# Kernel optimization log

Hardware: AMD Instinct MI355X
Metric: run time of the kernel (lower is better)

Reference implementation:

```python
import jax, jax.numpy as jnp
import numpy as np

NUM_EXPERTS = 8
TOP_K = 2
HIDDEN = 1024
INTER = 3584
BATCH = 2
SEQ = 2048
TOKENS = BATCH * SEQ


def setup_inputs() -> dict:
    key = jax.random.key(0)
    k_h, k_l, k_w1, k_w2, k_w3 = jax.random.split(key, 5)
    hidden_states = jax.random.normal(k_h, (TOKENS, HIDDEN), dtype=jnp.float32)
    # Router: top-2 over softmaxed logits, renormalized (standard Mixtral routing)
    logits = jax.random.normal(k_l, (TOKENS, NUM_EXPERTS), dtype=jnp.float32)
    probs = jax.nn.softmax(logits, axis=-1)
    routing_weights, selected = jax.lax.top_k(probs, TOP_K)  # [T, K], [T, K]
    routing_weights = routing_weights / jnp.sum(routing_weights, axis=-1, keepdims=True)
    # expert_mask: [num_experts, top_k, tokens]
    expert_mask = jax.nn.one_hot(selected, NUM_EXPERTS, dtype=jnp.int32).transpose(2, 1, 0)
    scale = 0.02
    w1 = jax.random.normal(k_w1, (NUM_EXPERTS, HIDDEN, INTER), dtype=jnp.float32) * scale
    w2 = jax.random.normal(k_w2, (NUM_EXPERTS, INTER, HIDDEN), dtype=jnp.float32) * scale
    w3 = jax.random.normal(k_w3, (NUM_EXPERTS, HIDDEN, INTER), dtype=jnp.float32) * scale
    return {
        "expert_mask": expert_mask,
        "hidden_states": hidden_states,
        "routing_weights": routing_weights,
        "w1": w1,
        "w2": w2,
        "w3": w3,
        "batch_size": BATCH,
        "sequence_length": SEQ,
        "hidden_dim": HIDDEN,
    }


def reference(expert_mask, hidden_states, routing_weights, w1, w2, w3,
              batch_size, sequence_length, hidden_dim):
    num_experts = w1.shape[0]
    tokens = batch_size * sequence_length
    # Extra row at the end absorbs writes from fill_value=-1 padding (as in source).
    final = jnp.zeros((tokens + 1, hidden_dim), dtype=hidden_states.dtype)
    for e in range(num_experts):
        # idx: which top-k slot; top_x: which token. Padded with -1.
        idx, top_x = jnp.nonzero(expert_mask[e], size=sequence_length, fill_value=-1)
        cur = hidden_states[top_x]  # [S, H]
        h = (jax.nn.silu(cur @ w1[e]) * (cur @ w3[e])) @ w2[e]  # SwiGLU MLP
        h = h * routing_weights[top_x, idx, None]
        final = final.at[top_x].set(h + final[top_x])
    final = final[:-1]
    return final.reshape(batch_size, sequence_length, hidden_dim)
```

## Files before the change

kernel.cpp:

```cpp
#include <hip/hip_runtime.h>
#include <hip/hip_bf16.h>
#include <cstdint>
#include <cstddef>

#define NEXP  8
#define NTOK  4096
#define HID   1024
#define INTER 3584
#define CAP   2048

#define BM  128
#define BN  128
#define BK  32

typedef __attribute__((ext_vector_type(4))) float floatx4;
typedef __attribute__((ext_vector_type(8))) short shortx8;
typedef unsigned short u16;

__device__ __forceinline__ u16 f2bf(float f) {
    union { float f; unsigned u; } v; v.f = f;
    unsigned r = v.u + 0x7fffu + ((v.u >> 16) & 1u);
    return (u16)(r >> 16);
}

__device__ __forceinline__ shortx8 pack8(const float* v) {
    shortx8 r;
#pragma unroll
    for (int i = 0; i < 8; ++i) r[i] = (short)f2bf(v[i]);
    return r;
}

__device__ __forceinline__ void async_ld16(const void* g, void* l) {
    __builtin_amdgcn_global_load_lds(
        (const __attribute__((address_space(1))) unsigned int*)g,
        (__attribute__((address_space(3))) unsigned int*)l, 16, 0, 0);
}

__global__ void route_kernel(const int* __restrict__ mask, const float* __restrict__ rw,
                             int* __restrict__ cnt, int* __restrict__ list,
                             float* __restrict__ wgt) {
    int t = blockIdx.x * blockDim.x + threadIdx.x;
    if (t >= NTOK) return;
#pragma unroll
    for (int e = 0; e < NEXP; ++e) {
#pragma unroll
        for (int k = 0; k < 2; ++k) {
            if (mask[(e * 2 + k) * NTOK + t] != 0) {
                int pos = atomicAdd(&cnt[e], 1);
                if (pos < CAP) {
                    list[e * CAP + pos] = t;
                    wgt[e * CAP + pos] = rw[t * 2 + k];
                }
            }
        }
    }
}

__global__ void xcvt_kernel(const float* __restrict__ X, u16* __restrict__ Xb) {
    const int i = (blockIdx.x * 256 + threadIdx.x) * 8;
    float4 a = *(const float4*)&X[i];
    float4 b = *(const float4*)&X[i + 4];
    float v[8] = {a.x, a.y, a.z, a.w, b.x, b.y, b.z, b.w};
    *(shortx8*)&Xb[i] = pack8(v);
}

__global__ void transpose_cvt_kernel(const float* __restrict__ src, u16* __restrict__ dst,
                                     int K, int N) {
    const int e = blockIdx.z;
    src += (size_t)e * K * N;
    dst += (size_t)e * K * N;
    const int n0 = blockIdx.x * 64;
    const int k0 = blockIdx.y * 64;
    __shared__ u16 lds[64 * 72];
    const int t  = threadIdx.x;
    const int rr = t >> 4;
    const int c4 = t & 15;
#pragma unroll
    for (int it = 0; it < 4; ++it) {
        const int r = it * 16 + rr;
        float4 f = *(const float4*)&src[(size_t)(k0 + r) * N + n0 + c4 * 4];
        lds[(c4 * 4 + 0) * 72 + r] = f2bf(f.x);
        lds[(c4 * 4 + 1) * 72 + r] = f2bf(f.y);
        lds[(c4 * 4 + 2) * 72 + r] = f2bf(f.z);
        lds[(c4 * 4 + 3) * 72 + r] = f2bf(f.w);
    }
    __syncthreads();
    const int row8 = t >> 3;
    const int col8 = t & 7;
#pragma unroll
    for (int it = 0; it < 2; ++it) {
        const int row = it * 32 + row8;
        *(shortx8*)&dst[(size_t)(n0 + row) * K + k0 + col8 * 8] =
            *(const shortx8*)&lds[row * 72 + col8 * 8];
    }
}

__global__ __launch_bounds__(256, 2)
void gemm1_kernel(const u16* __restrict__ Xb, const u16* __restrict__ W1b,
                  const u16* __restrict__ W3b, const int* __restrict__ cnt,
                  const int* __restrict__ list, const float* __restrict__ wgt,
                  u16* __restrict__ H) {
    const int e  = blockIdx.z;
    const int ce = min(cnt[e], CAP);
    const int m0 = blockIdx.y * BM;
    if (m0 >= ce) return;
    const int n0 = blockIdx.x * BN;

    __shared__ u16 lA [BM * BK];
    __shared__ u16 lB1[BN * BK];
    __shared__ u16 lB3[BN * BK];

    const int tid  = threadIdx.x;
    const int lane = tid & 63;
    const int wave = tid >> 6;

    const int srow0 = wave * 32 + (lane >> 2);
    const int srow1 = srow0 + 16;
    const int scol  = (lane & 3) * 8;
    const int lo0 = wave * 1024 + lane * 8;
    const int lo1 = lo0 + 512;

    const int t0 = list[e * CAP + min(m0 + srow0, ce - 1)];
    const int t1 = list[e * CAP + min(m0 + srow1, ce - 1)];
    const u16* ap0  = Xb + (size_t)t0 * HID + scol;
    const u16* ap1  = Xb + (size_t)t1 * HID + scol;
    const u16* b1p0 = W1b + ((size_t)e * INTER + n0 + srow0) * HID + scol;
    const u16* b1p1 = b1p0 + (size_t)16 * HID;
    const u16* b3p0 = W3b + ((size_t)e * INTER + n0 + srow0) * HID + scol;
    const u16* b3p1 = b3p0 + (size_t)16 * HID;

    const int fl = lane & 15, fq = lane >> 4;
    const int wm  = (wave >> 1) * 64;
    const int wnn = (wave & 1) * 64;

    floatx4 acc1[4][4], acc3[4][4];
#pragma unroll
    for (int i = 0; i < 4; ++i)
#pragma unroll
        for (int j = 0; j < 4; ++j)
#pragma unroll
            for (int r = 0; r < 4; ++r) { acc1[i][j][r] = 0.f; acc3[i][j][r] = 0.f; }

    for (int k0 = 0; k0 < HID; k0 += BK) {
        __syncthreads();
        async_ld16(ap0  + k0, &lA [lo0]);
        async_ld16(ap1  + k0, &lA [lo1]);
        async_ld16(b1p0 + k0, &lB1[lo0]);
        async_ld16(b1p1 + k0, &lB1[lo1]);
        async_ld16(b3p0 + k0, &lB3[lo0]);
        async_ld16(b3p1 + k0, &lB3[lo1]);
        __syncthreads();

        shortx8 af[4], b1f[4], b3f[4];
#pragma unroll
        for (int i = 0; i < 4; ++i)
            af[i] = *(const shortx8*)&lA[(wm + i * 16 + fl) * BK + fq * 8];
#pragma unroll
        for (int j = 0; j < 4; ++j) {
            b1f[j] = *(const shortx8*)&lB1[(wnn + j * 16 + fl) * BK + fq * 8];
            b3f[j] = *(const shortx8*)&lB3[(wnn + j * 16 + fl) * BK + fq * 8];
        }
#pragma unroll
        for (int i = 0; i < 4; ++i)
#pragma unroll
            for (int j = 0; j < 4; ++j) {
                acc1[i][j] = __builtin_amdgcn_mfma_f32_16x16x32_bf16(af[i], b1f[j], acc1[i][j], 0, 0, 0);
                acc3[i][j] = __builtin_amdgcn_mfma_f32_16x16x32_bf16(af[i], b3f[j], acc3[i][j], 0, 0, 0);
            }
    }

#pragma unroll
    for (int i = 0; i < 4; ++i) {
        const int rowb = m0 + wm + i * 16 + fq * 4;
#pragma unroll
        for (int r = 0; r < 4; ++r) {
            const int row = rowb + r;
            const bool valid = row < ce;
            const float rwv = valid ? wgt[e * CAP + row] : 0.f;
            u16* hp = H + (size_t)(e * CAP + (valid ? row : 0)) * INTER;
#pragma unroll
            for (int j = 0; j < 4; ++j) {
                const int col = n0 + wnn + j * 16 + fl;
                float h1 = acc1[i][j][r];
                float h3 = acc3[i][j][r];
                float sv = h1 / (1.f + __expf(-h1)) * h3 * rwv;
                if (valid) hp[col] = f2bf(sv);
            }
        }
    }
}

__global__ __launch_bounds__(256, 2)
void gemm2_kernel(const u16* __restrict__ H, const u16* __restrict__ W2b,
                  const int* __restrict__ cnt, const int* __restrict__ list,
                  float* __restrict__ out) {
    const int e  = blockIdx.z;
    const int ce = min(cnt[e], CAP);
    const int m0 = blockIdx.y * BM;
    if (m0 >= ce) return;
    const int n0 = blockIdx.x * BN;

    __shared__ u16 lA[BM * BK];
    __shared__ u16 lB[BN * BK];

    const int tid  = threadIdx.x;
    const int lane = tid & 63;
    const int wave = tid >> 6;

    const int srow0 = wave * 32 + (lane >> 2);
    const int srow1 = srow0 + 16;
    const int scol  = (lane & 3) * 8;
    const int lo0 = wave * 1024 + lane * 8;
    const int lo1 = lo0 + 512;

    const u16* ap0 = H + (size_t)(e * CAP + m0 + srow0) * INTER + scol;
    const u16* ap1 = ap0 + (size_t)16 * INTER;
    const u16* bp0 = W2b + ((size_t)e * HID + n0 + srow0) * INTER + scol;
    const u16* bp1 = bp0 + (size_t)16 * INTER;

    const int fl = lane & 15, fq = lane >> 4;
    const int wm  = (wave >> 1) * 64;
    const int wnn = (wave & 1) * 64;

    floatx4 acc[4][4];
#pragma unroll
    for (int i = 0; i < 4; ++i)
#pragma unroll
        for (int j = 0; j < 4; ++j)
#pragma unroll
            for (int r = 0; r < 4; ++r) acc[i][j][r] = 0.f;

    for (int k0 = 0; k0 < INTER; k0 += BK) {
        __syncthreads();
        async_ld16(ap0 + k0, &lA[lo0]);
        async_ld16(ap1 + k0, &lA[lo1]);
        async_ld16(bp0 + k0, &lB[lo0]);
        async_ld16(bp1 + k0, &lB[lo1]);
        __syncthreads();

        shortx8 af[4], bf[4];
#pragma unroll
        for (int i = 0; i < 4; ++i)
            af[i] = *(const shortx8*)&lA[(wm + i * 16 + fl) * BK + fq * 8];
#pragma unroll
        for (int j = 0; j < 4; ++j)
            bf[j] = *(const shortx8*)&lB[(wnn + j * 16 + fl) * BK + fq * 8];
#pragma unroll
        for (int i = 0; i < 4; ++i)
#pragma unroll
            for (int j = 0; j < 4; ++j)
                acc[i][j] = __builtin_amdgcn_mfma_f32_16x16x32_bf16(af[i], bf[j], acc[i][j], 0, 0, 0);
    }

#pragma unroll
    for (int i = 0; i < 4; ++i) {
        const int rowb = m0 + wm + i * 16 + fq * 4;
#pragma unroll
        for (int r = 0; r < 4; ++r) {
            const int row = rowb + r;
            const bool valid = row < ce;
            const int tok = valid ? list[e * CAP + row] : 0;
            float* op = out + (size_t)tok * HID;
#pragma unroll
            for (int j = 0; j < 4; ++j) {
                const int col = n0 + wnn + j * 16 + fl;
                if (valid) atomicAdd(&op[col], acc[i][j][r]);
            }
        }
    }
}

extern "C" void kernel_launch(void* const* d_in, const int* in_sizes, int n_in,
                              void* d_out, int out_size, void* d_ws, size_t ws_size,
                              hipStream_t stream) {
    const int*   mask = (const int*)  d_in[0];
    const float* X    = (const float*)d_in[1];
    const float* rw   = (const float*)d_in[2];
    const float* w1   = (const float*)d_in[3];
    const float* w2   = (const float*)d_in[4];
    const float* w3   = (const float*)d_in[5];
    float* out = (float*)d_out;

    char* ws = (char*)d_ws;
    size_t off = 0;
    int*   cnt  = (int*)(ws + off);  off += 256;
    int*   list = (int*)(ws + off);  off += (size_t)NEXP * CAP * 4;
    float* wgt  = (float*)(ws + off); off += (size_t)NEXP * CAP * 4;
    u16*   Xb   = (u16*)(ws + off);  off += (size_t)NTOK * HID * 2;
    u16*   W1b  = (u16*)(ws + off);  off += (size_t)NEXP * HID * INTER * 2;
    u16*   W3b  = (u16*)(ws + off);  off += (size_t)NEXP * HID * INTER * 2;
    u16*   W2b  = (u16*)(ws + off);  off += (size_t)NEXP * HID * INTER * 2;
    u16*   H    = (u16*)(ws + off);  off += (size_t)NEXP * CAP * INTER * 2;

    hipMemsetAsync(cnt, 0, 256, stream);
    hipMemsetAsync(d_out, 0, (size_t)out_size * sizeof(float), stream);

    route_kernel<<<dim3((NTOK + 255) / 256), dim3(256), 0, stream>>>(mask, rw, cnt, list, wgt);
    xcvt_kernel<<<dim3(NTOK * HID / (256 * 8)), dim3(256), 0, stream>>>(X, Xb);
    transpose_cvt_kernel<<<dim3(INTER / 64, HID / 64, NEXP), dim3(256), 0, stream>>>(w1, W1b, HID, INTER);
    transpose_cvt_kernel<<<dim3(INTER / 64, HID / 64, NEXP), dim3(256), 0, stream>>>(w3, W3b, HID, INTER);
    transpose_cvt_kernel<<<dim3(HID / 64, INTER / 64, NEXP), dim3(256), 0, stream>>>(w2, W2b, INTER, HID);

    gemm1_kernel<<<dim3(INTER / BN, CAP / BM, NEXP), dim3(256), 0, stream>>>(Xb, W1b, W3b, cnt, list, wgt, H);
    gemm2_kernel<<<dim3(HID / BN, CAP / BM, NEXP), dim3(256), 0, stream>>>(H, W2b, cnt, list, out);
}
```

Before: 722.8 us.

## Enlarge GEMM M-tile, XCD-aware block mapping, replace atomics with partials plus combine

The GEMM M-tile doubles to 256 rows and blocks grow to 512 threads (8 waves), so each weight tile is reused across more tokens. Blocks use a flattened grid that maps experts and column tiles onto XCDs for L2 locality. The scatter atomicAdd in gemm2 is replaced by plain stores into a per-slot partial buffer that aliases the W1b region, followed by a combine kernel that sums each token's two slots, which also drops the output memset. The weight transpose kernels are merged and pack two bf16 values per 32-bit LDS word. The aliasing of part onto W1b depends on W1b no longer being needed after gemm1, and the larger tiles raise register and LDS pressure.

```diff
diff --git a/kernel.cpp b/kernel.cpp
--- a/kernel.cpp
+++ b/kernel.cpp
@@ -9,13 +9,14 @@
 #define INTER 3584
 #define CAP   2048
 
-#define BM  128
+#define BM  256
 #define BN  128
 #define BK  32
 
 typedef __attribute__((ext_vector_type(4))) float floatx4;
 typedef __attribute__((ext_vector_type(8))) short shortx8;
 typedef unsigned short u16;
+typedef unsigned int   u32;
 
 __device__ __forceinline__ u16 f2bf(float f) {
     union { float f; unsigned u; } v; v.f = f;
@@ -38,7 +39,7 @@
 
 __global__ void route_kernel(const int* __restrict__ mask, const float* __restrict__ rw,
                              int* __restrict__ cnt, int* __restrict__ list,
-                             float* __restrict__ wgt) {
+                             float* __restrict__ wgt, int* __restrict__ slot) {
     int t = blockIdx.x * blockDim.x + threadIdx.x;
     if (t >= NTOK) return;
 #pragma unroll
@@ -50,6 +51,9 @@
                 if (pos < CAP) {
                     list[e * CAP + pos] = t;
                     wgt[e * CAP + pos] = rw[t * 2 + k];
+                    slot[t * 2 + k] = e * CAP + pos;
+                } else {
+                    slot[t * 2 + k] = -1;
                 }
             }
         }
@@ -64,47 +68,71 @@
     *(shortx8*)&Xb[i] = pack8(v);
 }
 
-__global__ void transpose_cvt_kernel(const float* __restrict__ src, u16* __restrict__ dst,
-                                     int K, int N) {
+__device__ __forceinline__ void tcvt_tile(const float* __restrict__ src, u16* __restrict__ dst,
+                                          int K, int N, int n0, int k0, u32* ldsT, int t) {
+    const int nc  = t & 15;
+    const int kp0 = t >> 4;
+#pragma unroll
+    for (int it = 0; it < 2; ++it) {
+        const int kp = kp0 + it * 16;
+        const int k  = kp * 2;
+        const float* s0 = src + (size_t)(k0 + k) * N + n0 + nc * 4;
+        float4 f0 = *(const float4*)s0;
+        float4 f1 = *(const float4*)(s0 + N);
+        ldsT[(nc * 4 + 0) * 33 + kp] = (u32)f2bf(f0.x) | ((u32)f2bf(f1.x) << 16);
+        ldsT[(nc * 4 + 1) * 33 + kp] = (u32)f2bf(f0.y) | ((u32)f2bf(f1.y) << 16);
+        ldsT[(nc * 4 + 2) * 33 + kp] = (u32)f2bf(f0.z) | ((u32)f2bf(f1.z) << 16);
+        ldsT[(nc * 4 + 3) * 33 + kp] = (u32)f2bf(f0.w) | ((u32)f2bf(f1.w) << 16);
+    }
+    __syncthreads();
+    const int rr = t >> 3;
+    const int c  = t & 7;
+#pragma unroll
+    for (int it = 0; it < 2; ++it) {
+        const int n = rr + it * 32;
+        const u32* p = &ldsT[n * 33 + c * 4];
+        u32 v0 = p[0], v1 = p[1], v2 = p[2], v3 = p[3];
+        u32* d = (u32*)&dst[(size_t)(n0 + n) * K + k0 + c * 8];
+        d[0] = v0; d[1] = v1; d[2] = v2; d[3] = v3;
+    }
+}
+
+__global__ __launch_bounds__(256)
+void tcvt13_kernel(const float* __restrict__ w1, const float* __restrict__ w3,
+                   u16* __restrict__ W1b, u16* __restrict__ W3b) {
+    __shared__ u32 ldsT[64 * 33];
+    const int z = blockIdx.z;
+    const int e = z >> 1;
+    const float* src = ((z & 1) ? w3 : w1) + (size_t)e * HID * INTER;
+    u16*         dst = ((z & 1) ? W3b : W1b) + (size_t)e * HID * INTER;
+    tcvt_tile(src, dst, HID, INTER, blockIdx.x * 64, blockIdx.y * 64, ldsT, threadIdx.x);
+}
+
+__global__ __launch_bounds__(256)
+void tcvt2_kernel(const float* __restrict__ w2, u16* __restrict__ W2b) {
+    __shared__ u32 ldsT[64 * 33];
     const int e = blockIdx.z;
-    src += (size_t)e * K * N;
-    dst += (size_t)e * K * N;
-    const int n0 = blockIdx.x * 64;
-    const int k0 = blockIdx.y * 64;
-    __shared__ u16 lds[64 * 72];
-    const int t  = threadIdx.x;
-    const int rr = t >> 4;
-    const int c4 = t & 15;
-#pragma unroll
-    for (int it = 0; it < 4; ++it) {
-        const int r = it * 16 + rr;
-        float4 f = *(const float4*)&src[(size_t)(k0 + r) * N + n0 + c4 * 4];
-        lds[(c4 * 4 + 0) * 72 + r] = f2bf(f.x);
-        lds[(c4 * 4 + 1) * 72 + r] = f2bf(f.y);
-        lds[(c4 * 4 + 2) * 72 + r] = f2bf(f.z);
-        lds[(c4 * 4 + 3) * 72 + r] = f2bf(f.w);
-    }
-    __syncthreads();
-    const int row8 = t >> 3;
-    const int col8 = t & 7;
-#pragma unroll
-    for (int it = 0; it < 2; ++it) {
-        const int row = it * 32 + row8;
-        *(shortx8*)&dst[(size_t)(n0 + row) * K + k0 + col8 * 8] =
-            *(const shortx8*)&lds[row * 72 + col8 * 8];
-    }
-}
-
-__global__ __launch_bounds__(256, 2)
+    tcvt_tile(w2 + (size_t)e * INTER * HID, W2b + (size_t)e * INTER * HID,
+              INTER, HID, blockIdx.x * 64, blockIdx.y * 64, ldsT, threadIdx.x);
+}
+
+__global__ __launch_bounds__(512, 2)
 void gemm1_kernel(const u16* __restrict__ Xb, const u16* __restrict__ W1b,
                   const u16* __restrict__ W3b, const int* __restrict__ cnt,
                   const int* __restrict__ list, const float* __restrict__ wgt,
                   u16* __restrict__ H) {
-    const int e  = blockIdx.z;
-    const int ce = min(cnt[e], CAP);
-    const int m0 = blockIdx.y * BM;
+    const int f = blockIdx.x;
+    const int xcd = f & 7;
+    const int u   = f >> 3;
+    const int mb  = u & 7;
+    const int p   = u >> 3;
+    const int pair = xcd * 28 + p;
+    const int nb  = pair % 28;
+    const int e   = pair / 28;
+    const int ce  = min(cnt[e], CAP);
+    const int m0  = mb * BM;
     if (m0 >= ce) return;
-    const int n0 = blockIdx.x * BN;
+    const int n0  = nb * BN;
 
     __shared__ u16 lA [BM * BK];
     __shared__ u16 lB1[BN * BK];
@@ -113,21 +141,20 @@
     const int tid  = threadIdx.x;
     const int lane = tid & 63;
     const int wave = tid >> 6;
-
-    const int srow0 = wave * 32 + (lane >> 2);
-    const int srow1 = srow0 + 16;
-    const int scol  = (lane & 3) * 8;
-    const int lo0 = wave * 1024 + lane * 8;
-    const int lo1 = lo0 + 512;
-
-    const int t0 = list[e * CAP + min(m0 + srow0, ce - 1)];
-    const int t1 = list[e * CAP + min(m0 + srow1, ce - 1)];
-    const u16* ap0  = Xb + (size_t)t0 * HID + scol;
-    const u16* ap1  = Xb + (size_t)t1 * HID + scol;
-    const u16* b1p0 = W1b + ((size_t)e * INTER + n0 + srow0) * HID + scol;
-    const u16* b1p1 = b1p0 + (size_t)16 * HID;
-    const u16* b3p0 = W3b + ((size_t)e * INTER + n0 + srow0) * HID + scol;
-    const u16* b3p1 = b3p0 + (size_t)16 * HID;
+    const int rsub = lane >> 2;
+    const int scol = (lane & 3) * 8;
+
+    const int arow0 = wave * 32 + rsub;
+    const int aoff0 = wave * 1024 + lane * 8;
+    const int aoff1 = aoff0 + 512;
+    const int t0 = list[e * CAP + min(m0 + arow0, ce - 1)];
+    const int t1 = list[e * CAP + min(m0 + arow0 + 16, ce - 1)];
+    const u16* ap0 = Xb + (size_t)t0 * HID + scol;
+    const u16* ap1 = Xb + (size_t)t1 * HID + scol;
+    const int brow = wave * 16 + rsub;
+    const int boff = wave * 512 + lane * 8;
+    const u16* b1p = W1b + ((size_t)e * INTER + n0 + brow) * HID + scol;
+    const u16* b3p = W3b + ((size_t)e * INTER + n0 + brow) * HID + scol;
 
     const int fl = lane & 15, fq = lane >> 4;
     const int wm  = (wave >> 1) * 64;
@@ -143,12 +170,10 @@
 
     for (int k0 = 0; k0 < HID; k0 += BK) {
         __syncthreads();
-        async_ld16(ap0  + k0, &lA [lo0]);
-        async_ld16(ap1  + k0, &lA [lo1]);
-        async_ld16(b1p0 + k0, &lB1[lo0]);
-        async_ld16(b1p1 + k0, &lB1[lo1]);
-        async_ld16(b3p0 + k0, &lB3[lo0]);
-        async_ld16(b3p1 + k0, &lB3[lo1]);
+        async_ld16(ap0 + k0, &lA [aoff0]);
+        async_ld16(ap1 + k0, &lA [aoff1]);
+        async_ld16(b1p + k0, &lB1[boff]);
+        async_ld16(b3p + k0, &lB3[boff]);
         __syncthreads();
 
         shortx8 af[4], b1f[4], b3f[4];
@@ -190,15 +215,21 @@
     }
 }
 
-__global__ __launch_bounds__(256, 2)
+__global__ __launch_bounds__(512, 2)
 void gemm2_kernel(const u16* __restrict__ H, const u16* __restrict__ W2b,
-                  const int* __restrict__ cnt, const int* __restrict__ list,
-                  float* __restrict__ out) {
-    const int e  = blockIdx.z;
-    const int ce = min(cnt[e], CAP);
-    const int m0 = blockIdx.y * BM;
+                  const int* __restrict__ cnt, float* __restrict__ part) {
+    const int f = blockIdx.x;
+    const int xcd = f & 7;
+    const int u   = f >> 3;
+    const int mb  = u & 7;
+    const int p   = u >> 3;
+    const int pair = xcd * 8 + p;
+    const int nb  = pair & 7;
+    const int e   = pair >> 3;
+    const int ce  = min(cnt[e], CAP);
+    const int m0  = mb * BM;
     if (m0 >= ce) return;
-    const int n0 = blockIdx.x * BN;
+    const int n0  = nb * BN;
 
     __shared__ u16 lA[BM * BK];
     __shared__ u16 lB[BN * BK];
@@ -206,17 +237,17 @@
     const int tid  = threadIdx.x;
     const int lane = tid & 63;
     const int wave = tid >> 6;
-
-    const int srow0 = wave * 32 + (lane >> 2);
-    const int srow1 = srow0 + 16;
-    const int scol  = (lane & 3) * 8;
-    const int lo0 = wave * 1024 + lane * 8;
-    const int lo1 = lo0 + 512;
-
-    const u16* ap0 = H + (size_t)(e * CAP + m0 + srow0) * INTER + scol;
+    const int rsub = lane >> 2;
+    const int scol = (lane & 3) * 8;
+
+    const int arow0 = wave * 32 + rsub;
+    const int aoff0 = wave * 1024 + lane * 8;
+    const int aoff1 = aoff0 + 512;
+    const u16* ap0 = H + (size_t)(e * CAP + m0 + arow0) * INTER + scol;
     const u16* ap1 = ap0 + (size_t)16 * INTER;
-    const u16* bp0 = W2b + ((size_t)e * HID + n0 + srow0) * INTER + scol;
-    const u16* bp1 = bp0 + (size_t)16 * INTER;
+    const int brow = wave * 16 + rsub;
+    const int boff = wave * 512 + lane * 8;
+    const u16* bp = W2b + ((size_t)e * HID + n0 + brow) * INTER + scol;
 
     const int fl = lane & 15, fq = lane >> 4;
     const int wm  = (wave >> 1) * 64;
@@ -232,10 +263,9 @@
 
     for (int k0 = 0; k0 < INTER; k0 += BK) {
         __syncthreads();
-        async_ld16(ap0 + k0, &lA[lo0]);
-        async_ld16(ap1 + k0, &lA[lo1]);
-        async_ld16(bp0 + k0, &lB[lo0]);
-        async_ld16(bp1 + k0, &lB[lo1]);
+        async_ld16(ap0 + k0, &lA[aoff0]);
+        async_ld16(ap1 + k0, &lA[aoff1]);
+        async_ld16(bp  + k0, &lB[boff]);
         __syncthreads();
 
         shortx8 af[4], bf[4];
@@ -259,15 +289,33 @@
         for (int r = 0; r < 4; ++r) {
             const int row = rowb + r;
             const bool valid = row < ce;
-            const int tok = valid ? list[e * CAP + row] : 0;
-            float* op = out + (size_t)tok * HID;
+            float* pp = part + (size_t)(e * CAP + row) * HID;
 #pragma unroll
             for (int j = 0; j < 4; ++j) {
                 const int col = n0 + wnn + j * 16 + fl;
-                if (valid) atomicAdd(&op[col], acc[i][j][r]);
+                if (valid) pp[col] = acc[i][j][r];
             }
         }
     }
+}
+
+__global__ void combine_kernel(const float* __restrict__ part, const int* __restrict__ slot,
+                               float* __restrict__ out) {
+    const int gid = blockIdx.x * 256 + threadIdx.x;
+    const int t = gid >> 8;
+    const int h = (gid & 255) * 4;
+    const int s0 = slot[t * 2];
+    const int s1 = slot[t * 2 + 1];
+    float4 r = make_float4(0.f, 0.f, 0.f, 0.f);
+    if (s0 >= 0) {
+        float4 a = *(const float4*)&part[(size_t)s0 * HID + h];
+        r.x += a.x; r.y += a.y; r.z += a.z; r.w += a.w;
+    }
+    if (s1 >= 0) {
+        float4 b = *(const float4*)&part[(size_t)s1 * HID + h];
+        r.x += b.x; r.y += b.y; r.z += b.z; r.w += b.w;
+    }
+    *(float4*)&out[(size_t)t * HID + h] = r;
 }
 
 extern "C" void kernel_launch(void* const* d_in, const int* in_sizes, int n_in,
@@ -283,24 +331,27 @@
 
     char* ws = (char*)d_ws;
     size_t off = 0;
-    int*   cnt  = (int*)(ws + off);  off += 256;
-    int*   list = (int*)(ws + off);  off += (size_t)NEXP * CAP * 4;
+    int*   cnt  = (int*)(ws + off);   off += 256;
+    int*   list = (int*)(ws + off);   off += (size_t)NEXP * CAP * 4;
     float* wgt  = (float*)(ws + off); off += (size_t)NEXP * CAP * 4;
-    u16*   Xb   = (u16*)(ws + off);  off += (size_t)NTOK * HID * 2;
-    u16*   W1b  = (u16*)(ws + off);  off += (size_t)NEXP * HID * INTER * 2;
-    u16*   W3b  = (u16*)(ws + off);  off += (size_t)NEXP * HID * INTER * 2;
-    u16*   W2b  = (u16*)(ws + off);  off += (size_t)NEXP * HID * INTER * 2;
-    u16*   H    = (u16*)(ws + off);  off += (size_t)NEXP * CAP * INTER * 2;
+    int*   slot = (int*)(ws + off);   off += (size_t)NTOK * 2 * 4;
+    u16*   Xb   = (u16*)(ws + off);   off += (size_t)NTOK * HID * 2;
+    u16*   W1b  = (u16*)(ws + off);   off += (size_t)NEXP * HID * INTER * 2;
+    u16*   W3b  = (u16*)(ws + off);   off += (size_t)NEXP * HID * INTER * 2;
+    u16*   W2b  = (u16*)(ws + off);   off += (size_t)NEXP * HID * INTER * 2;
+    u16*   H    = (u16*)(ws + off);   off += (size_t)NEXP * CAP * INTER * 2;
+    float* part = (float*)W1b;
 
     hipMemsetAsync(cnt, 0, 256, stream);
-    hipMemsetAsync(d_out, 0, (size_t)out_size * sizeof(float), stream);
-
-    route_kernel<<<dim3((NTOK + 255) / 256), dim3(256), 0, stream>>>(mask, rw, cnt, list, wgt);
+
+    route_kernel<<<dim3((NTOK + 255) / 256), dim3(256), 0, stream>>>(mask, rw, cnt, list, wgt, slot);
     xcvt_kernel<<<dim3(NTOK * HID / (256 * 8)), dim3(256), 0, stream>>>(X, Xb);
-    transpose_cvt_kernel<<<dim3(INTER / 64, HID / 64, NEXP), dim3(256), 0, stream>>>(w1, W1b, HID, INTER);
-    transpose_cvt_kernel<<<dim3(INTER / 64, HID / 64, NEXP), dim3(256), 0, stream>>>(w3, W3b, HID, INTER);
-    transpose_cvt_kernel<<<dim3(HID / 64, INTER / 64, NEXP), dim3(256), 0, stream>>>(w2, W2b, INTER, HID);
-
-    gemm1_kernel<<<dim3(INTER / BN, CAP / BM, NEXP), dim3(256), 0, stream>>>(Xb, W1b, W3b, cnt, list, wgt, H);
-    gemm2_kernel<<<dim3(HID / BN, CAP / BM, NEXP), dim3(256), 0, stream>>>(H, W2b, cnt, list, out);
-}
+    tcvt13_kernel<<<dim3(INTER / 64, HID / 64, NEXP * 2), dim3(256), 0, stream>>>(w1, w3, W1b, W3b);
+    tcvt2_kernel<<<dim3(HID / 64, INTER / 64, NEXP), dim3(256), 0, stream>>>(w2, W2b);
+
+    gemm1_kernel<<<dim3(NEXP * (INTER / BN) * (CAP / BM)), dim3(512), 0, stream>>>(
+        Xb, W1b, W3b, cnt, list, wgt, H);
+    gemm2_kernel<<<dim3(NEXP * (HID / BN) * (CAP / BM)), dim3(512), 0, stream>>>(
+        H, W2b, cnt, part);
+    combine_kernel<<<dim3(NTOK), dim3(256), 0, stream>>>(part, slot, out);
+}
```

Measured after the change: 834.7 us. +15.5%, slower.
